# Performance work log

Hardware: AMD Instinct MI355X
Metric: run time of the kernel (lower is better)

## Reference

```python
import jax, jax.numpy as jnp
import numpy as np

N = 8192
F_IN = 1024
F_OUT = 256
ALPHA = 0.2          # LeakyReLU negative slope
ADJ_DENSITY = 0.004  # pre-symmetrization edge probability -> avg degree ~65
NEG_INF = -9.0e15    # matches -9000000000000000.0 in the torch code


def setup_inputs() -> dict:
    key = jax.random.key(0)
    k_h, k_W, k_a, k_adj = jax.random.split(key, 4)
    h = jax.random.normal(k_h, (N, F_IN), dtype=jnp.float32)
    # xavier_uniform with gain=1.414
    lim_W = 1.414 * np.sqrt(6.0 / (F_IN + F_OUT))
    W = jax.random.uniform(k_W, (F_IN, F_OUT), dtype=jnp.float32, minval=-lim_W, maxval=lim_W)
    lim_a = 1.414 * np.sqrt(6.0 / (2 * F_OUT + 1))
    a = jax.random.uniform(k_a, (2 * F_OUT, 1), dtype=jnp.float32, minval=-lim_a, maxval=lim_a)
    # sparse symmetric 0/1 adjacency (float, like the torch code's dense adj)
    u = jax.random.uniform(k_adj, (N, N))
    m = u < ADJ_DENSITY
    adj = (m | m.T).astype(jnp.float32)
    return {"h": h, "adj": adj, "W": W, "a": a}


def reference(h, adj, W, a):
    # --- GAT attention ---
    Wh = h @ W                                   # [N, F_OUT]
    Wh1 = Wh @ a[:F_OUT]                          # [N, 1]
    Wh2 = Wh @ a[F_OUT:]                          # [N, 1]
    e = jax.nn.leaky_relu(Wh1 + Wh2.T, negative_slope=ALPHA)   # [N, N]
    attention = jax.nn.softmax(jnp.where(adj > 0, e, NEG_INF), axis=1)

    # --- per-row variable-k pruning of attention + attention@attention.T ---
    n = adj.shape[0]
    diag = jnp.eye(n, dtype=bool)
    adj_nodiag = jnp.where(diag, 0.0, adj)
    s2 = jnp.count_nonzero(adj_nodiag, axis=1)    # [N] int, variable k per row

    attention2step = attention @ attention.T      # [N, N] dense GEMM
    comb = attention + attention2step
    comb = jnp.where(diag, 0.0, comb)

    # threshold = s2[i]-th largest value of row i (np.partition(row, -k)[-k])
    sorted_desc = -jnp.sort(-comb, axis=1)        # [N, N] descending per row
    idx = jnp.maximum(s2 - 1, 0)[:, None]         # clamp for s2==0 rows
    thr = jnp.take_along_axis(sorted_desc, idx, axis=1)   # [N, 1]
    # keep values >= threshold (torch code zeros values strictly < partition);
    # rows with s2 == 0 are zeroed entirely
    pruned = jnp.where((s2[:, None] > 0) & (comb >= thr), comb, 0.0)
    adj_resize = (pruned > 0).astype(jnp.float32)

    # --- output (eval mode: dropout is identity); concat=True -> ELU ---
    h_prime = attention @ Wh                      # [N, F_OUT]
    return jax.nn.elu(h_prime), adj_resize
```

## Files before the change

### kernel.cpp

```cpp
#include <hip/hip_runtime.h>
#include <cstdint>
#include <cstddef>

#define NN 8192
#define KFIN 1024
#define KFOUT 256
#define MAXD 192
#define LRALPHA 0.2f

typedef float f32x4 __attribute__((ext_vector_type(4)));

__global__ void __launch_bounds__(256) k_build_csr(
    const float* __restrict__ adj, int* __restrict__ nbr,
    int* __restrict__ deg, int* __restrict__ s2v) {
  const int wave = threadIdx.x >> 6;
  const int lane = threadIdx.x & 63;
  const int row = blockIdx.x * 4 + wave;
  const float* arow = adj + (size_t)row * NN;
  int* outp = nbr + (size_t)row * MAXD;
  int count = 0;
  int dflag = 0;
  const unsigned long long below = (1ull << lane) - 1ull;
  for (int c0 = 0; c0 < NN; c0 += 256) {
    const int c = c0 + lane * 4;
    const f32x4 v = __builtin_nontemporal_load(
        reinterpret_cast<const f32x4*>(arow + c));
    const unsigned long long m0 = __ballot(v[0] > 0.0f);
    const unsigned long long m1 = __ballot(v[1] > 0.0f);
    const unsigned long long m2 = __ballot(v[2] > 0.0f);
    const unsigned long long m3 = __ballot(v[3] > 0.0f);
    int pos = count + (int)(__popcll(m0 & below) + __popcll(m1 & below) +
                            __popcll(m2 & below) + __popcll(m3 & below));
    if (v[0] > 0.0f) { if (pos < MAXD) outp[pos] = c + 0; ++pos; if (c + 0 == row) dflag = 1; }
    if (v[1] > 0.0f) { if (pos < MAXD) outp[pos] = c + 1; ++pos; if (c + 1 == row) dflag = 1; }
    if (v[2] > 0.0f) { if (pos < MAXD) outp[pos] = c + 2; ++pos; if (c + 2 == row) dflag = 1; }
    if (v[3] > 0.0f) { if (pos < MAXD) outp[pos] = c + 3; ++pos; if (c + 3 == row) dflag = 1; }
    count += (int)(__popcll(m0) + __popcll(m1) + __popcll(m2) + __popcll(m3));
  }
  const int anyd = __any(dflag) ? 1 : 0;
  if (lane == 0) {
    deg[row] = count < MAXD ? count : MAXD;
    s2v[row] = count - anyd;
  }
}

__global__ void __launch_bounds__(256) k_gemm(
    const float* __restrict__ A, const float* __restrict__ B,
    float* __restrict__ C) {
  __shared__ float As[32][65];
  __shared__ float Bs[32][65];
  const int tid = threadIdx.x;
  const int brow = blockIdx.y * 64;
  const int bcol = blockIdx.x * 64;
  const int tx = tid & 15;
  const int ty = tid >> 4;
  float acc[4][4];
#pragma unroll
  for (int i = 0; i < 4; ++i)
#pragma unroll
    for (int j = 0; j < 4; ++j) acc[i][j] = 0.0f;
  const int ar = tid >> 2;
  const int ac = (tid & 3) << 2;
  const int br = tid >> 4;
  const int bc = (tid & 15) << 2;
  for (int k0 = 0; k0 < KFIN; k0 += 32) {
    const float4 av0 =
        *reinterpret_cast<const float4*>(A + (size_t)(brow + ar) * KFIN + k0 + ac);
    const float4 av1 =
        *reinterpret_cast<const float4*>(A + (size_t)(brow + ar) * KFIN + k0 + 16 + ac);
    const float4 bv0 =
        *reinterpret_cast<const float4*>(B + (size_t)(k0 + br) * KFOUT + bcol + bc);
    const float4 bv1 =
        *reinterpret_cast<const float4*>(B + (size_t)(k0 + 16 + br) * KFOUT + bcol + bc);
    As[ac + 0][ar] = av0.x;
    As[ac + 1][ar] = av0.y;
    As[ac + 2][ar] = av0.z;
    As[ac + 3][ar] = av0.w;
    As[16 + ac + 0][ar] = av1.x;
    As[16 + ac + 1][ar] = av1.y;
    As[16 + ac + 2][ar] = av1.z;
    As[16 + ac + 3][ar] = av1.w;
    Bs[br][bc + 0] = bv0.x;
    Bs[br][bc + 1] = bv0.y;
    Bs[br][bc + 2] = bv0.z;
    Bs[br][bc + 3] = bv0.w;
    Bs[16 + br][bc + 0] = bv1.x;
    Bs[16 + br][bc + 1] = bv1.y;
    Bs[16 + br][bc + 2] = bv1.z;
    Bs[16 + br][bc + 3] = bv1.w;
    __syncthreads();
#pragma unroll
    for (int kk = 0; kk < 32; ++kk) {
      const float a0 = As[kk][ty * 4 + 0];
      const float a1 = As[kk][ty * 4 + 1];
      const float a2 = As[kk][ty * 4 + 2];
      const float a3 = As[kk][ty * 4 + 3];
      const float b0 = Bs[kk][tx * 4 + 0];
      const float b1 = Bs[kk][tx * 4 + 1];
      const float b2 = Bs[kk][tx * 4 + 2];
      const float b3 = Bs[kk][tx * 4 + 3];
      acc[0][0] += a0 * b0; acc[0][1] += a0 * b1; acc[0][2] += a0 * b2; acc[0][3] += a0 * b3;
      acc[1][0] += a1 * b0; acc[1][1] += a1 * b1; acc[1][2] += a1 * b2; acc[1][3] += a1 * b3;
      acc[2][0] += a2 * b0; acc[2][1] += a2 * b1; acc[2][2] += a2 * b2; acc[2][3] += a2 * b3;
      acc[3][0] += a3 * b0; acc[3][1] += a3 * b1; acc[3][2] += a3 * b2; acc[3][3] += a3 * b3;
    }
    __syncthreads();
  }
#pragma unroll
  for (int i = 0; i < 4; ++i) {
#pragma unroll
    for (int j = 0; j < 4; ++j) {
      C[(size_t)(brow + ty * 4 + i) * KFOUT + bcol + tx * 4 + j] = acc[i][j];
    }
  }
}

__global__ void __launch_bounds__(256) k_rowdots(
    const float* __restrict__ Wh, const float* __restrict__ a,
    float* __restrict__ Wh1, float* __restrict__ Wh2) {
  __shared__ float sA[256];
  __shared__ float sB[256];
  const int row = blockIdx.x;
  const int t = threadIdx.x;
  const float w = Wh[(size_t)row * KFOUT + t];
  sA[t] = w * a[t];
  sB[t] = w * a[KFOUT + t];
  __syncthreads();
  for (int s = 128; s > 0; s >>= 1) {
    if (t < s) {
      sA[t] += sA[t + s];
      sB[t] += sB[t + s];
    }
    __syncthreads();
  }
  if (t == 0) {
    Wh1[row] = sA[0];
    Wh2[row] = sB[0];
  }
}

__global__ void __launch_bounds__(256) k_stats(
    const int* __restrict__ nbr, const int* __restrict__ deg,
    const float* __restrict__ Wh1, const float* __restrict__ Wh2,
    float* __restrict__ mrow, float* __restrict__ Zrow,
    float* __restrict__ att, short* __restrict__ qb8) {
  const int wave = threadIdx.x >> 6;
  const int lane = threadIdx.x & 63;
  const int row = blockIdx.x * 4 + wave;
  const int d = deg[row];
  const size_t rowbase = (size_t)row * MAXD;
  const int* cols = nbr + rowbase;
  const float w1 = Wh1[row];
  int c0 = 0x7fffffff, c1 = 0x7fffffff, c2 = 0x7fffffff;
  float e0 = -1e30f, e1 = -1e30f, e2 = -1e30f;
  const bool a0 = lane < d, a1 = lane + 64 < d, a2 = lane + 128 < d;
  if (a0) { c0 = cols[lane];       float x = w1 + Wh2[c0]; e0 = x > 0.0f ? x : LRALPHA * x; }
  if (a1) { c1 = cols[lane + 64];  float x = w1 + Wh2[c1]; e1 = x > 0.0f ? x : LRALPHA * x; }
  if (a2) { c2 = cols[lane + 128]; float x = w1 + Wh2[c2]; e2 = x > 0.0f ? x : LRALPHA * x; }
  float mx = fmaxf(e0, fmaxf(e1, e2));
  for (int o = 32; o > 0; o >>= 1) mx = fmaxf(mx, __shfl_xor(mx, o));
  const float x0 = a0 ? expf(e0 - mx) : 0.0f;
  const float x1 = a1 ? expf(e1 - mx) : 0.0f;
  const float x2 = a2 ? expf(e2 - mx) : 0.0f;
  float sum = x0 + x1 + x2;
  for (int o = 32; o > 0; o >>= 1) sum += __shfl_xor(sum, o);
  const float Z = (d > 0) ? sum : 1.0f;
  const float invZ = 1.0f / Z;
  if (a0) att[rowbase + lane] = x0 * invZ;
  if (a1) att[rowbase + lane + 64] = x1 * invZ;
  if (a2) att[rowbase + lane + 128] = x2 * invZ;
  int b[7] = {0, 0, 0, 0, 0, 0, 0};
#pragma unroll
  for (int m = 1; m <= 7; ++m) {
    b[m - 1] = (int)__popcll(__ballot(a0 && c0 < m * 1024)) +
               (int)__popcll(__ballot(a1 && c1 < m * 1024)) +
               (int)__popcll(__ballot(a2 && c2 < m * 1024));
  }
  if (lane == 0) {
    mrow[row] = mx;
    Zrow[row] = Z;
    short* q = qb8 + (size_t)row * 8;
    q[0] = (short)b[0]; q[1] = (short)b[1]; q[2] = (short)b[2]; q[3] = (short)b[3];
    q[4] = (short)b[4]; q[5] = (short)b[5]; q[6] = (short)b[6]; q[7] = (short)d;
  }
}

__global__ void __launch_bounds__(256) k_att(
    const int* __restrict__ nbr, const int* __restrict__ deg,
    const float* __restrict__ Wh1, const float* __restrict__ Wh2,
    const float* __restrict__ mrow, const float* __restrict__ Zrow,
    int2* __restrict__ edgesT) {
  const int wave = threadIdx.x >> 6;
  const int lane = threadIdx.x & 63;
  const int row = blockIdx.x * 4 + wave;
  const int d = deg[row];
  const size_t rowbase = (size_t)row * MAXD;
  const int* cols = nbr + rowbase;
  const float w2r = Wh2[row];
  for (int t = lane; t < d; t += 64) {
    const int j = cols[t];
    float e2 = Wh1[j] + w2r;
    e2 = e2 > 0.0f ? e2 : LRALPHA * e2;
    const float v = expf(e2 - mrow[j]) / Zrow[j];
    edgesT[rowbase + t] = make_int2(j, __float_as_int(v));
  }
}

__global__ void __launch_bounds__(512) k_twostep(
    const int* __restrict__ nbr, const int* __restrict__ deg,
    const int* __restrict__ s2v, const float* __restrict__ att,
    const int2* __restrict__ edgesT, const short* __restrict__ qb8,
    float* __restrict__ out1) {
  __shared__ float comb[NN];
  __shared__ float wvals[MAXD];
  __shared__ unsigned short kcols[MAXD];
  __shared__ short sqb[MAXD][8];
  __shared__ unsigned int hist[256];
  __shared__ unsigned int scomp[512];
  __shared__ unsigned int shPrefix;
  __shared__ int shRemaining;
  __shared__ int shNc;
  const int tid = threadIdx.x;
  const int wave = tid >> 6;
  const int lane = tid & 63;
  const int row = blockIdx.x;
  const f32x4 z4 = {0.0f, 0.0f, 0.0f, 0.0f};
  for (int j = tid * 4; j < NN; j += 2048)
    *reinterpret_cast<f32x4*>(&comb[j]) = z4;
  const int d = deg[row];
  const int* cols = nbr + (size_t)row * MAXD;
  const float* arow = att + (size_t)row * MAXD;
  for (int t = tid; t < d; t += 512) {
    const int c = cols[t];
    kcols[t] = (unsigned short)c;
    wvals[t] = arow[t];
    *reinterpret_cast<int4*>(&sqb[t][0]) =
        *reinterpret_cast<const int4*>(&qb8[(size_t)c * 8]);
  }
  if (tid == 0) shNc = 0;
  __syncthreads();
  {
    const int grp = lane >> 3;
    const int sub = lane & 7;
    for (int t0 = 0; t0 < d; t0 += 8) {
      const int t = t0 + grp;
      if (t < d) {
        const int qs = wave ? (int)sqb[t][wave - 1] : 0;
        const int qe = (int)sqb[t][wave];
        const float w = wvals[t];
        const int2* ek = edgesT + (size_t)kcols[t] * MAXD;
        for (int off = qs + sub; off < qe; off += 8) {
          const int2 e = ek[off];
          atomicAdd(&comb[e.x], w * __int_as_float(e.y));
        }
      }
    }
  }
  {
    const short* qr = qb8 + (size_t)row * 8;
    const int qlo = wave ? (int)qr[wave - 1] : 0;
    const int qhi = (int)qr[wave];
    for (int t = qlo + lane; t < qhi; t += 64) comb[(int)kcols[t]] += wvals[t];
  }
  __syncthreads();
  if (tid == 0) comb[row] = 0.0f;
  __syncthreads();
  const int kk = s2v[row];
  const size_t obase = (size_t)row * NN;
  if (kk <= 0) {
    for (int j = tid * 4; j < NN; j += 2048)
      __builtin_nontemporal_store(z4, reinterpret_cast<f32x4*>(&out1[obase + j]));
    return;
  }
  if (tid < 256) hist[tid] = 0u;
  __syncthreads();
  for (int j = tid * 4; j < NN; j += 2048) {
    const f32x4 cv = *reinterpret_cast<const f32x4*>(&comb[j]);
#pragma unroll
    for (int q = 0; q < 4; ++q) {
      const unsigned int u = __float_as_uint(cv[q]);
      if (u != 0u) atomicAdd(&hist[u >> 24], 1u);
    }
  }
  __syncthreads();
  if (tid < 64) {
    const int bHi = 255 - 4 * lane;
    const unsigned int c0 = hist[bHi];
    const unsigned int c1 = hist[bHi - 1];
    const unsigned int c2 = hist[bHi - 2];
    const unsigned int c3 = hist[bHi - 3];
    const unsigned int gs = c0 + c1 + c2 + c3;
    unsigned int run2 = gs;
    for (int o = 1; o < 64; o <<= 1) {
      const unsigned int tt = __shfl_up(run2, o);
      if (lane >= o) run2 += tt;
    }
    const unsigned int pre = run2 - gs;
    const unsigned int rem = (unsigned int)kk;
    if (pre < rem && pre + gs >= rem) {
      unsigned int above;
      int digit;
      if (pre + c0 >= rem) { digit = bHi; above = pre; }
      else if (pre + c0 + c1 >= rem) { digit = bHi - 1; above = pre + c0; }
      else if (pre + c0 + c1 + c2 >= rem) { digit = bHi - 2; above = pre + c0 + c1; }
      else { digit = bHi - 3; above = pre + c0 + c1 + c2; }
      shPrefix = (unsigned)digit << 24;
      shRemaining = kk - (int)above;
    }
  }
  __syncthreads();
  unsigned int prefix = shPrefix;
  int remaining = shRemaining;
  const unsigned int digit0 = prefix >> 24;
  __syncthreads();
  for (int j = tid * 4; j < NN; j += 2048) {
    const f32x4 cv = *reinterpret_cast<const f32x4*>(&comb[j]);
#pragma unroll
    for (int q = 0; q < 4; ++q) {
      const unsigned int u = __float_as_uint(cv[q]);
      if (u != 0u && (u >> 24) == digit0) {
        const int idx = atomicAdd(&shNc, 1);
        if (idx < 512) scomp[idx] = u;
      }
    }
  }
  __syncthreads();
  const int nc = shNc;
  const bool densefb = nc > 512;
  const unsigned int myu = (!densefb && tid < nc) ? scomp[tid] : 0u;
  for (int pass = 1; pass < 4; ++pass) {
    const int shift = 24 - 8 * pass;
    const unsigned int pmask = 0xFFFFFFFFu << (shift + 8);
    if (tid < 256) hist[tid] = 0u;
    __syncthreads();
    if (!densefb) {
      if (tid < nc && (myu & pmask) == prefix)
        atomicAdd(&hist[(myu >> shift) & 255u], 1u);
    } else {
      for (int j = tid * 4; j < NN; j += 2048) {
        const f32x4 cv = *reinterpret_cast<const f32x4*>(&comb[j]);
#pragma unroll
        for (int q = 0; q < 4; ++q) {
          const unsigned int u = __float_as_uint(cv[q]);
          if (u != 0u && (u & pmask) == prefix)
            atomicAdd(&hist[(u >> shift) & 255u], 1u);
        }
      }
    }
    __syncthreads();
    if (tid < 64) {
      const int bHi = 255 - 4 * lane;
      const unsigned int c0 = hist[bHi];
      const unsigned int c1 = hist[bHi - 1];
      const unsigned int c2 = hist[bHi - 2];
      const unsigned int c3 = hist[bHi - 3];
      const unsigned int gs = c0 + c1 + c2 + c3;
      unsigned int run2 = gs;
      for (int o = 1; o < 64; o <<= 1) {
        const unsigned int tt = __shfl_up(run2, o);
        if (lane >= o) run2 += tt;
      }
      const unsigned int pre = run2 - gs;
      const unsigned int rem = (unsigned int)remaining;
      if (pre < rem && pre + gs >= rem) {
        unsigned int above;
        int digit;
        if (pre + c0 >= rem) { digit = bHi; above = pre; }
        else if (pre + c0 + c1 >= rem) { digit = bHi - 1; above = pre + c0; }
        else if (pre + c0 + c1 + c2 >= rem) { digit = bHi - 2; above = pre + c0 + c1; }
        else { digit = bHi - 3; above = pre + c0 + c1 + c2; }
        shPrefix = prefix | ((unsigned int)digit << shift);
        shRemaining = remaining - (int)above;
      }
    }
    __syncthreads();
    prefix = shPrefix;
    remaining = shRemaining;
    __syncthreads();
  }
  const float thr = __uint_as_float(prefix);
  for (int j = tid * 4; j < NN; j += 2048) {
    const f32x4 cv = *reinterpret_cast<const f32x4*>(&comb[j]);
    f32x4 ov;
    ov[0] = (cv[0] >= thr && cv[0] > 0.0f) ? 1.0f : 0.0f;
    ov[1] = (cv[1] >= thr && cv[1] > 0.0f) ? 1.0f : 0.0f;
    ov[2] = (cv[2] >= thr && cv[2] > 0.0f) ? 1.0f : 0.0f;
    ov[3] = (cv[3] >= thr && cv[3] > 0.0f) ? 1.0f : 0.0f;
    __builtin_nontemporal_store(ov, reinterpret_cast<f32x4*>(&out1[obase + j]));
  }
}

__global__ void __launch_bounds__(256) k_hprime(
    const int* __restrict__ nbr, const int* __restrict__ deg,
    const float* __restrict__ att, const float* __restrict__ Wh,
    float* __restrict__ out0) {
  __shared__ int scol[MAXD];
  __shared__ float sval[MAXD];
  const int row = blockIdx.x;
  const int c = threadIdx.x;
  const int d = deg[row];
  const int* cols = nbr + (size_t)row * MAXD;
  const float* arow = att + (size_t)row * MAXD;
  for (int t = threadIdx.x; t < d; t += 256) {
    scol[t] = cols[t];
    sval[t] = arow[t];
  }
  __syncthreads();
  float a0 = 0.0f, a1 = 0.0f, a2 = 0.0f, a3 = 0.0f;
  int t = 0;
  for (; t + 4 <= d; t += 4) {
    a0 += sval[t + 0] * Wh[(size_t)scol[t + 0] * KFOUT + c];
    a1 += sval[t + 1] * Wh[(size_t)scol[t + 1] * KFOUT + c];
    a2 += sval[t + 2] * Wh[(size_t)scol[t + 2] * KFOUT + c];
    a3 += sval[t + 3] * Wh[(size_t)scol[t + 3] * KFOUT + c];
  }
  for (; t < d; ++t) a0 += sval[t] * Wh[(size_t)scol[t] * KFOUT + c];
  const float acc = (a0 + a1) + (a2 + a3);
  out0[(size_t)row * KFOUT + c] = acc > 0.0f ? acc : expm1f(acc);
}

extern "C" void kernel_launch(void* const* d_in, const int* in_sizes, int n_in,
                              void* d_out, int out_size, void* d_ws, size_t ws_size,
                              hipStream_t stream) {
  const float* h = (const float*)d_in[0];
  const float* adj = (const float*)d_in[1];
  const float* W = (const float*)d_in[2];
  const float* a = (const float*)d_in[3];

  float* out0 = (float*)d_out;
  float* out1 = out0 + (size_t)NN * KFOUT;

  float* Wh = (float*)d_ws;
  float* Wh1 = Wh + (size_t)NN * KFOUT;
  float* Wh2 = Wh1 + NN;
  float* mrow = Wh2 + NN;
  float* Zrow = mrow + NN;
  float* att = Zrow + NN;
  float* edgesF = att + (size_t)NN * MAXD;
  int2* edgesT = (int2*)edgesF;
  int* nbr = (int*)(edgesF + (size_t)NN * MAXD * 2);
  int* deg = nbr + (size_t)NN * MAXD;
  int* s2v = deg + NN;
  short* qb8 = (short*)(s2v + NN);

  k_build_csr<<<NN / 4, 256, 0, stream>>>(adj, nbr, deg, s2v);
  dim3 ggrid(KFOUT / 64, NN / 64);
  k_gemm<<<ggrid, 256, 0, stream>>>(h, W, Wh);
  k_rowdots<<<NN, 256, 0, stream>>>(Wh, a, Wh1, Wh2);
  k_stats<<<NN / 4, 256, 0, stream>>>(nbr, deg, Wh1, Wh2, mrow, Zrow, att, qb8);
  k_att<<<NN / 4, 256, 0, stream>>>(nbr, deg, Wh1, Wh2, mrow, Zrow, edgesT);
  k_twostep<<<NN, 512, 0, stream>>>(nbr, deg, s2v, att, edgesT, qb8, out1);
  k_hprime<<<NN, 256, 0, stream>>>(nbr, deg, att, Wh, out0);
}
```

Measured before the change: 474.5 us.

## Fuse h' aggregation into twostep kernel, wave-level rowdots, pack softmax stats

Moves the attention@Wh aggregation and ELU from a separate kernel into k_twostep, which already stages the row's neighbour columns and weights in shared memory. The two thread halves each accumulate partial sums that are combined through reused shared memory. k_rowdots now computes one row per wave with float4 loads and shuffle reductions instead of a shared-memory tree. The softmax max and reciprocal of Z are packed into one float2, so the k_att division becomes a multiply. This removes one launch and a redundant CSR reload, at the cost of more registers and work per twostep block.

```diff
diff --git a/kernel.cpp b/kernel.cpp
--- a/kernel.cpp
+++ b/kernel.cpp
@@ -118,32 +118,29 @@
 __global__ void __launch_bounds__(256) k_rowdots(
     const float* __restrict__ Wh, const float* __restrict__ a,
     float* __restrict__ Wh1, float* __restrict__ Wh2) {
-  __shared__ float sA[256];
-  __shared__ float sB[256];
-  const int row = blockIdx.x;
-  const int t = threadIdx.x;
-  const float w = Wh[(size_t)row * KFOUT + t];
-  sA[t] = w * a[t];
-  sB[t] = w * a[KFOUT + t];
-  __syncthreads();
-  for (int s = 128; s > 0; s >>= 1) {
-    if (t < s) {
-      sA[t] += sA[t + s];
-      sB[t] += sB[t + s];
-    }
-    __syncthreads();
-  }
-  if (t == 0) {
-    Wh1[row] = sA[0];
-    Wh2[row] = sB[0];
+  const int wave = threadIdx.x >> 6;
+  const int lane = threadIdx.x & 63;
+  const int row = blockIdx.x * 4 + wave;
+  const float4 w = *reinterpret_cast<const float4*>(Wh + (size_t)row * KFOUT + lane * 4);
+  const float4 aA = *reinterpret_cast<const float4*>(a + lane * 4);
+  const float4 aB = *reinterpret_cast<const float4*>(a + KFOUT + lane * 4);
+  float sA = w.x * aA.x + w.y * aA.y + w.z * aA.z + w.w * aA.w;
+  float sB = w.x * aB.x + w.y * aB.y + w.z * aB.z + w.w * aB.w;
+  for (int o = 32; o > 0; o >>= 1) {
+    sA += __shfl_xor(sA, o);
+    sB += __shfl_xor(sB, o);
+  }
+  if (lane == 0) {
+    Wh1[row] = sA;
+    Wh2[row] = sB;
   }
 }
 
 __global__ void __launch_bounds__(256) k_stats(
     const int* __restrict__ nbr, const int* __restrict__ deg,
     const float* __restrict__ Wh1, const float* __restrict__ Wh2,
-    float* __restrict__ mrow, float* __restrict__ Zrow,
-    float* __restrict__ att, short* __restrict__ qb8) {
+    float2* __restrict__ mz, float* __restrict__ att,
+    short* __restrict__ qb8) {
   const int wave = threadIdx.x >> 6;
   const int lane = threadIdx.x & 63;
   const int row = blockIdx.x * 4 + wave;
@@ -177,8 +174,7 @@
                (int)__popcll(__ballot(a2 && c2 < m * 1024));
   }
   if (lane == 0) {
-    mrow[row] = mx;
-    Zrow[row] = Z;
+    mz[row] = make_float2(mx, invZ);
     short* q = qb8 + (size_t)row * 8;
     q[0] = (short)b[0]; q[1] = (short)b[1]; q[2] = (short)b[2]; q[3] = (short)b[3];
     q[4] = (short)b[4]; q[5] = (short)b[5]; q[6] = (short)b[6]; q[7] = (short)d;
@@ -188,8 +184,7 @@
 __global__ void __launch_bounds__(256) k_att(
     const int* __restrict__ nbr, const int* __restrict__ deg,
     const float* __restrict__ Wh1, const float* __restrict__ Wh2,
-    const float* __restrict__ mrow, const float* __restrict__ Zrow,
-    int2* __restrict__ edgesT) {
+    const float2* __restrict__ mz, int2* __restrict__ edgesT) {
   const int wave = threadIdx.x >> 6;
   const int lane = threadIdx.x & 63;
   const int row = blockIdx.x * 4 + wave;
@@ -201,7 +196,8 @@
     const int j = cols[t];
     float e2 = Wh1[j] + w2r;
     e2 = e2 > 0.0f ? e2 : LRALPHA * e2;
-    const float v = expf(e2 - mrow[j]) / Zrow[j];
+    const float2 m = mz[j];
+    const float v = expf(e2 - m.x) * m.y;
     edgesT[rowbase + t] = make_int2(j, __float_as_int(v));
   }
 }
@@ -210,7 +206,8 @@
     const int* __restrict__ nbr, const int* __restrict__ deg,
     const int* __restrict__ s2v, const float* __restrict__ att,
     const int2* __restrict__ edgesT, const short* __restrict__ qb8,
-    float* __restrict__ out1) {
+    const float* __restrict__ Wh, float* __restrict__ out1,
+    float* __restrict__ out0) {
   __shared__ float comb[NN];
   __shared__ float wvals[MAXD];
   __shared__ unsigned short kcols[MAXD];
@@ -239,6 +236,21 @@
   }
   if (tid == 0) shNc = 0;
   __syncthreads();
+  float hpacc;
+  {
+    const int c = tid & 255;
+    const int half = tid >> 8;
+    float p0 = 0.0f, p1 = 0.0f, p2 = 0.0f, p3 = 0.0f;
+    int t = half;
+    for (; t + 6 < d; t += 8) {
+      p0 += wvals[t]     * Wh[(size_t)kcols[t]     * KFOUT + c];
+      p1 += wvals[t + 2] * Wh[(size_t)kcols[t + 2] * KFOUT + c];
+      p2 += wvals[t + 4] * Wh[(size_t)kcols[t + 4] * KFOUT + c];
+      p3 += wvals[t + 6] * Wh[(size_t)kcols[t + 6] * KFOUT + c];
+    }
+    for (; t < d; t += 2) p0 += wvals[t] * Wh[(size_t)kcols[t] * KFOUT + c];
+    hpacc = (p0 + p1) + (p2 + p3);
+  }
   {
     const int grp = lane >> 3;
     const int sub = lane & 7;
@@ -263,6 +275,8 @@
     for (int t = qlo + lane; t < qhi; t += 64) comb[(int)kcols[t]] += wvals[t];
   }
   __syncthreads();
+  float* hp = reinterpret_cast<float*>(&sqb[0][0]);
+  hp[tid] = hpacc;
   if (tid == 0) comb[row] = 0.0f;
   __syncthreads();
   const int kk = s2v[row];
@@ -270,81 +284,15 @@
   if (kk <= 0) {
     for (int j = tid * 4; j < NN; j += 2048)
       __builtin_nontemporal_store(z4, reinterpret_cast<f32x4*>(&out1[obase + j]));
-    return;
-  }
-  if (tid < 256) hist[tid] = 0u;
-  __syncthreads();
-  for (int j = tid * 4; j < NN; j += 2048) {
-    const f32x4 cv = *reinterpret_cast<const f32x4*>(&comb[j]);
-#pragma unroll
-    for (int q = 0; q < 4; ++q) {
-      const unsigned int u = __float_as_uint(cv[q]);
-      if (u != 0u) atomicAdd(&hist[u >> 24], 1u);
-    }
-  }
-  __syncthreads();
-  if (tid < 64) {
-    const int bHi = 255 - 4 * lane;
-    const unsigned int c0 = hist[bHi];
-    const unsigned int c1 = hist[bHi - 1];
-    const unsigned int c2 = hist[bHi - 2];
-    const unsigned int c3 = hist[bHi - 3];
-    const unsigned int gs = c0 + c1 + c2 + c3;
-    unsigned int run2 = gs;
-    for (int o = 1; o < 64; o <<= 1) {
-      const unsigned int tt = __shfl_up(run2, o);
-      if (lane >= o) run2 += tt;
-    }
-    const unsigned int pre = run2 - gs;
-    const unsigned int rem = (unsigned int)kk;
-    if (pre < rem && pre + gs >= rem) {
-      unsigned int above;
-      int digit;
-      if (pre + c0 >= rem) { digit = bHi; above = pre; }
-      else if (pre + c0 + c1 >= rem) { digit = bHi - 1; above = pre + c0; }
-      else if (pre + c0 + c1 + c2 >= rem) { digit = bHi - 2; above = pre + c0 + c1; }
-      else { digit = bHi - 3; above = pre + c0 + c1 + c2; }
-      shPrefix = (unsigned)digit << 24;
-      shRemaining = kk - (int)above;
-    }
-  }
-  __syncthreads();
-  unsigned int prefix = shPrefix;
-  int remaining = shRemaining;
-  const unsigned int digit0 = prefix >> 24;
-  __syncthreads();
-  for (int j = tid * 4; j < NN; j += 2048) {
-    const f32x4 cv = *reinterpret_cast<const f32x4*>(&comb[j]);
-#pragma unroll
-    for (int q = 0; q < 4; ++q) {
-      const unsigned int u = __float_as_uint(cv[q]);
-      if (u != 0u && (u >> 24) == digit0) {
-        const int idx = atomicAdd(&shNc, 1);
-        if (idx < 512) scomp[idx] = u;
-      }
-    }
-  }
-  __syncthreads();
-  const int nc = shNc;
-  const bool densefb = nc > 512;
-  const unsigned int myu = (!densefb && tid < nc) ? scomp[tid] : 0u;
-  for (int pass = 1; pass < 4; ++pass) {
-    const int shift = 24 - 8 * pass;
-    const unsigned int pmask = 0xFFFFFFFFu << (shift + 8);
+  } else {
     if (tid < 256) hist[tid] = 0u;
     __syncthreads();
-    if (!densefb) {
-      if (tid < nc && (myu & pmask) == prefix)
-        atomicAdd(&hist[(myu >> shift) & 255u], 1u);
-    } else {
-      for (int j = tid * 4; j < NN; j += 2048) {
-        const f32x4 cv = *reinterpret_cast<const f32x4*>(&comb[j]);
-#pragma unroll
-        for (int q = 0; q < 4; ++q) {
-          const unsigned int u = __float_as_uint(cv[q]);
-          if (u != 0u && (u & pmask) == prefix)
-            atomicAdd(&hist[(u >> shift) & 255u], 1u);
-        }
+    for (int j = tid * 4; j < NN; j += 2048) {
+      const f32x4 cv = *reinterpret_cast<const f32x4*>(&comb[j]);
+#pragma unroll
+      for (int q = 0; q < 4; ++q) {
+        const unsigned int u = __float_as_uint(cv[q]);
+        if (u != 0u) atomicAdd(&hist[u >> 24], 1u);
       }
     }
     __syncthreads();
@@ -361,7 +309,7 @@
         if (lane >= o) run2 += tt;
       }
       const unsigned int pre = run2 - gs;
-      const unsigned int rem = (unsigned int)remaining;
+      const unsigned int rem = (unsigned int)kk;
       if (pre < rem && pre + gs >= rem) {
         unsigned int above;
         int digit;
@@ -369,54 +317,96 @@
         else if (pre + c0 + c1 >= rem) { digit = bHi - 1; above = pre + c0; }
         else if (pre + c0 + c1 + c2 >= rem) { digit = bHi - 2; above = pre + c0 + c1; }
         else { digit = bHi - 3; above = pre + c0 + c1 + c2; }
-        shPrefix = prefix | ((unsigned int)digit << shift);
-        shRemaining = remaining - (int)above;
-      }
-    }
-    __syncthreads();
-    prefix = shPrefix;
-    remaining = shRemaining;
-    __syncthreads();
-  }
-  const float thr = __uint_as_float(prefix);
-  for (int j = tid * 4; j < NN; j += 2048) {
-    const f32x4 cv = *reinterpret_cast<const f32x4*>(&comb[j]);
-    f32x4 ov;
-    ov[0] = (cv[0] >= thr && cv[0] > 0.0f) ? 1.0f : 0.0f;
-    ov[1] = (cv[1] >= thr && cv[1] > 0.0f) ? 1.0f : 0.0f;
-    ov[2] = (cv[2] >= thr && cv[2] > 0.0f) ? 1.0f : 0.0f;
-    ov[3] = (cv[3] >= thr && cv[3] > 0.0f) ? 1.0f : 0.0f;
-    __builtin_nontemporal_store(ov, reinterpret_cast<f32x4*>(&out1[obase + j]));
-  }
-}
-
-__global__ void __launch_bounds__(256) k_hprime(
-    const int* __restrict__ nbr, const int* __restrict__ deg,
-    const float* __restrict__ att, const float* __restrict__ Wh,
-    float* __restrict__ out0) {
-  __shared__ int scol[MAXD];
-  __shared__ float sval[MAXD];
-  const int row = blockIdx.x;
-  const int c = threadIdx.x;
-  const int d = deg[row];
-  const int* cols = nbr + (size_t)row * MAXD;
-  const float* arow = att + (size_t)row * MAXD;
-  for (int t = threadIdx.x; t < d; t += 256) {
-    scol[t] = cols[t];
-    sval[t] = arow[t];
-  }
-  __syncthreads();
-  float a0 = 0.0f, a1 = 0.0f, a2 = 0.0f, a3 = 0.0f;
-  int t = 0;
-  for (; t + 4 <= d; t += 4) {
-    a0 += sval[t + 0] * Wh[(size_t)scol[t + 0] * KFOUT + c];
-    a1 += sval[t + 1] * Wh[(size_t)scol[t + 1] * KFOUT + c];
-    a2 += sval[t + 2] * Wh[(size_t)scol[t + 2] * KFOUT + c];
-    a3 += sval[t + 3] * Wh[(size_t)scol[t + 3] * KFOUT + c];
-  }
-  for (; t < d; ++t) a0 += sval[t] * Wh[(size_t)scol[t] * KFOUT + c];
-  const float acc = (a0 + a1) + (a2 + a3);
-  out0[(size_t)row * KFOUT + c] = acc > 0.0f ? acc : expm1f(acc);
+        shPrefix = (unsigned)digit << 24;
+        shRemaining = kk - (int)above;
+      }
+    }
+    __syncthreads();
+    unsigned int prefix = shPrefix;
+    int remaining = shRemaining;
+    const unsigned int digit0 = prefix >> 24;
+    __syncthreads();
+    for (int j = tid * 4; j < NN; j += 2048) {
+      const f32x4 cv = *reinterpret_cast<const f32x4*>(&comb[j]);
+#pragma unroll
+      for (int q = 0; q < 4; ++q) {
+        const unsigned int u = __float_as_uint(cv[q]);
+        if (u != 0u && (u >> 24) == digit0) {
+          const int idx = atomicAdd(&shNc, 1);
+          if (idx < 512) scomp[idx] = u;
+        }
+      }
+    }
+    __syncthreads();
+    const int nc = shNc;
+    const bool densefb = nc > 512;
+    const unsigned int myu = (!densefb && tid < nc) ? scomp[tid] : 0u;
+    for (int pass = 1; pass < 4; ++pass) {
+      const int shift = 24 - 8 * pass;
+      const unsigned int pmask = 0xFFFFFFFFu << (shift + 8);
+      if (tid < 256) hist[tid] = 0u;
+      __syncthreads();
+      if (!densefb) {
+        if (tid < nc && (myu & pmask) == prefix)
+          atomicAdd(&hist[(myu >> shift) & 255u], 1u);
+      } else {
+        for (int j = tid * 4; j < NN; j += 2048) {
+          const f32x4 cv = *reinterpret_cast<const f32x4*>(&comb[j]);
+#pragma unroll
+          for (int q = 0; q < 4; ++q) {
+            const unsigned int u = __float_as_uint(cv[q]);
+            if (u != 0u && (u & pmask) == prefix)
+              atomicAdd(&hist[(u >> shift) & 255u], 1u);
+          }
+        }
+      }
+      __syncthreads();
+      if (tid < 64) {
+        const int bHi = 255 - 4 * lane;
+        const unsigned int c0 = hist[bHi];
+        const unsigned int c1 = hist[bHi - 1];
+        const unsigned int c2 = hist[bHi - 2];
+        const unsigned int c3 = hist[bHi - 3];
+        const unsigned int gs = c0 + c1 + c2 + c3;
+        unsigned int run2 = gs;
+        for (int o = 1; o < 64; o <<= 1) {
+          const unsigned int tt = __shfl_up(run2, o);
+          if (lane >= o) run2 += tt;
+        }
+        const unsigned int pre = run2 - gs;
+        const unsigned int rem = (unsigned int)remaining;
+        if (pre < rem && pre + gs >= rem) {
+          unsigned int above;
+          int digit;
+          if (pre + c0 >= rem) { digit = bHi; above = pre; }
+          else if (pre + c0 + c1 >= rem) { digit = bHi - 1; above = pre + c0; }
+          else if (pre + c0 + c1 + c2 >= rem) { digit = bHi - 2; above = pre + c0 + c1; }
+          else { digit = bHi - 3; above = pre + c0 + c1 + c2; }
+          shPrefix = prefix | ((unsigned int)digit << shift);
+          shRemaining = remaining - (int)above;
+        }
+      }
+      __syncthreads();
+      prefix = shPrefix;
+      remaining = shRemaining;
+      __syncthreads();
+    }
+    const float thr = __uint_as_float(prefix);
+    for (int j = tid * 4; j < NN; j += 2048) {
+      const f32x4 cv = *reinterpret_cast<const f32x4*>(&comb[j]);
+      f32x4 ov;
+      ov[0] = (cv[0] >= thr && cv[0] > 0.0f) ? 1.0f : 0.0f;
+      ov[1] = (cv[1] >= thr && cv[1] > 0.0f) ? 1.0f : 0.0f;
+      ov[2] = (cv[2] >= thr && cv[2] > 0.0f) ? 1.0f : 0.0f;
+      ov[3] = (cv[3] >= thr && cv[3] > 0.0f) ? 1.0f : 0.0f;
+      __builtin_nontemporal_store(ov, reinterpret_cast<f32x4*>(&out1[obase + j]));
+    }
+  }
+  if (tid < 256) {
+    const float acc = hp[tid] + hp[tid + 256];
+    const float r = acc > 0.0f ? acc : expm1f(acc);
+    __builtin_nontemporal_store(r, &out0[(size_t)row * KFOUT + tid]);
+  }
 }
 
 extern "C" void kernel_launch(void* const* d_in, const int* in_sizes, int n_in,
@@ -442,13 +432,14 @@
   int* deg = nbr + (size_t)NN * MAXD;
   int* s2v = deg + NN;
   short* qb8 = (short*)(s2v + NN);
+  float2* mz = (float2*)(qb8 + (size_t)NN * 8);
 
   k_build_csr<<<NN / 4, 256, 0, stream>>>(adj, nbr, deg, s2v);
   dim3 ggrid(KFOUT / 64, NN / 64);
   k_gemm<<<ggrid, 256, 0, stream>>>(h, W, Wh);
-  k_rowdots<<<NN, 256, 0, stream>>>(Wh, a, Wh1, Wh2);
-  k_stats<<<NN / 4, 256, 0, stream>>>(nbr, deg, Wh1, Wh2, mrow, Zrow, att, qb8);
-  k_att<<<NN / 4, 256, 0, stream>>>(nbr, deg, Wh1, Wh2, mrow, Zrow, edgesT);
-  k_twostep<<<NN, 512, 0, stream>>>(nbr, deg, s2v, att, edgesT, qb8, out1);
-  k_hprime<<<NN, 256, 0, stream>>>(nbr, deg, att, Wh, out0);
-}
+  k_rowdots<<<NN / 4, 256, 0, stream>>>(Wh, a, Wh1, Wh2);
+  k_stats<<<NN / 4, 256, 0, stream>>>(nbr, deg, Wh1, Wh2, mz, att, qb8);
+  k_att<<<NN / 4, 256, 0, stream>>>(nbr, deg, Wh1, Wh2, mz, edgesT);
+  k_twostep<<<NN, 512, 0, stream>>>(nbr, deg, s2v, att, edgesT, qb8, Wh,
+                                    out1, out0);
+}
```

Measured after the change: 462.4 us. -2.5%, faster.
